# Optimization experiments

Hardware: AMD Instinct MI355X
Metric: run time of the kernel (lower is better)

The kernel has to match this reference:

```python
import jax, jax.numpy as jnp
import numpy as np

N, E, IN = 100000, 1600000, 128
H, C = 4, 16            # heads, out_channels
HID = H * C             # concat output dim = 64
SLOPE = 0.2             # GATv2Conv negative_slope default
EPS = 1e-5              # LayerNorm eps


def setup_inputs() -> dict:
    key = jax.random.key(0)
    ks = jax.random.split(key, 12)
    s = 0.05
    x = jax.random.normal(ks[0], (N, IN), jnp.float32)
    edge_index = jax.random.randint(ks[1], (2, E), 0, N, dtype=jnp.int32)
    return {
        "x": x,
        "edge_index": edge_index,
        # GATv2Conv params (lin_l: source, lin_r: target; both with bias)
        "W_l": jax.random.normal(ks[2], (IN, HID), jnp.float32) * s,
        "b_l": jnp.zeros((HID,), jnp.float32),
        "W_r": jax.random.normal(ks[3], (IN, HID), jnp.float32) * s,
        "b_r": jnp.zeros((HID,), jnp.float32),
        "att": jax.random.normal(ks[4], (H, C), jnp.float32) * s,
        "bias": jnp.zeros((HID,), jnp.float32),
        # residual projection Linear(in, heads*out, bias=False)
        "W_res": jax.random.normal(ks[5], (IN, HID), jnp.float32) * s,
        # pyg LayerNorm affine params
        "ln_w": jnp.ones((HID,), jnp.float32),
        "ln_b": jnp.zeros((HID,), jnp.float32),
    }


def reference(x, edge_index, W_l, b_l, W_r, b_r, att, bias, W_res, ln_w, ln_b):
    n = x.shape[0]
    # GATv2Conv adds self-loops by default
    loops = jnp.arange(n, dtype=edge_index.dtype)
    src = jnp.concatenate([edge_index[0], loops])  # message source j
    dst = jnp.concatenate([edge_index[1], loops])  # message target i

    xl = (x @ W_l + b_l).reshape(n, H, C)  # source-side projection
    xr = (x @ W_r + b_r).reshape(n, H, C)  # target-side projection

    # GATv2 attention: e_ij = att . LeakyReLU(xl_j + xr_i)
    e = jax.nn.leaky_relu(xl[src] + xr[dst], SLOPE)   # [Et, H, C]
    score = jnp.einsum('ehc,hc->eh', e, att)          # [Et, H]

    # segment softmax over incoming edges of each target node
    smax = jax.ops.segment_max(score, dst, num_segments=n)
    ex = jnp.exp(score - smax[dst])
    ssum = jax.ops.segment_sum(ex, dst, num_segments=n)
    alpha = ex / (ssum[dst] + 1e-16)                  # [Et, H]

    # weighted scatter-add of source features, concat heads
    msg = xl[src] * alpha[..., None]                  # [Et, H, C]
    out = jax.ops.segment_sum(msg, dst, num_segments=n).reshape(n, HID)
    out = out + bias + x @ W_res                      # bias + residual

    # pyg.nn.LayerNorm(mode='graph', batch=None): global mean/std over all elems
    out = out - out.mean()
    out = out / (out.std() + EPS)
    return out * ln_w + ln_b
```

## Files before the change

### kernel.cpp

```cpp
#include <hip/hip_runtime.h>
#include <math.h>

#define SLOPE  0.2f
#define LN_EPS 1e-5f
#define HID    64
#define IN_DIM 128
#define BM     64

__global__ __launch_bounds__(256) void proj_kernel(
    const float* __restrict__ x,
    const float* __restrict__ Wl, const float* __restrict__ bl,
    const float* __restrict__ Wr, const float* __restrict__ br,
    const float* __restrict__ Wres,
    float* __restrict__ xl, float* __restrict__ xr, float* __restrict__ out_un,
    int n)
{
    __shared__ float xs[BM][132];
    int t = threadIdx.x;
    int row0 = blockIdx.x * BM;

#pragma unroll
    for (int p = 0; p < 8; ++p) {
        int f  = t + p * 256;
        int r  = f >> 5;
        int c4 = f & 31;
        float4 v = make_float4(0.f, 0.f, 0.f, 0.f);
        if (row0 + r < n) v = ((const float4*)x)[(long)(row0 + r) * 32 + c4];
        *(float4*)&xs[r][c4 * 4] = v;
    }
    __syncthreads();

    int cb = (t & 15) * 4;
    int ry = (t >> 4) * 4;

    float4 acc[3][4];
#pragma unroll
    for (int r = 0; r < 4; ++r) {
        acc[0][r] = *(const float4*)&bl[cb];
        acc[1][r] = *(const float4*)&br[cb];
        acc[2][r] = make_float4(0.f, 0.f, 0.f, 0.f);
    }

    for (int k4 = 0; k4 < 32; ++k4) {
        float4 xv[4];
#pragma unroll
        for (int r = 0; r < 4; ++r)
            xv[r] = *(const float4*)&xs[ry + r][k4 * 4];
#pragma unroll
        for (int kk = 0; kk < 4; ++kk) {
            int k = k4 * 4 + kk;
            float4 w0 = *(const float4*)&Wl  [k * HID + cb];
            float4 w1 = *(const float4*)&Wr  [k * HID + cb];
            float4 w2 = *(const float4*)&Wres[k * HID + cb];
#pragma unroll
            for (int r = 0; r < 4; ++r) {
                float xvk = (kk == 0) ? xv[r].x : (kk == 1) ? xv[r].y
                          : (kk == 2) ? xv[r].z : xv[r].w;
                acc[0][r].x = fmaf(xvk, w0.x, acc[0][r].x);
                acc[0][r].y = fmaf(xvk, w0.y, acc[0][r].y);
                acc[0][r].z = fmaf(xvk, w0.z, acc[0][r].z);
                acc[0][r].w = fmaf(xvk, w0.w, acc[0][r].w);
                acc[1][r].x = fmaf(xvk, w1.x, acc[1][r].x);
                acc[1][r].y = fmaf(xvk, w1.y, acc[1][r].y);
                acc[1][r].z = fmaf(xvk, w1.z, acc[1][r].z);
                acc[1][r].w = fmaf(xvk, w1.w, acc[1][r].w);
                acc[2][r].x = fmaf(xvk, w2.x, acc[2][r].x);
                acc[2][r].y = fmaf(xvk, w2.y, acc[2][r].y);
                acc[2][r].z = fmaf(xvk, w2.z, acc[2][r].z);
                acc[2][r].w = fmaf(xvk, w2.w, acc[2][r].w);
            }
        }
    }

#pragma unroll
    for (int r = 0; r < 4; ++r) {
        long ro = row0 + ry + r;
        if (ro < n) {
            *(float4*)&xl    [ro * HID + cb] = acc[0][r];
            *(float4*)&xr    [ro * HID + cb] = acc[1][r];
            *(float4*)&out_un[ro * HID + cb] = acc[2][r];
        }
    }
}

__global__ void deg_init_kernel(int* __restrict__ deg, int n) {
    for (int i = blockIdx.x * blockDim.x + threadIdx.x; i < n; i += gridDim.x * blockDim.x)
        deg[i] = 1;
}

__global__ void deg_count_kernel(const int* __restrict__ dst, int* __restrict__ deg, int e) {
    for (int i = blockIdx.x * blockDim.x + threadIdx.x; i < e; i += gridDim.x * blockDim.x)
        atomicAdd(&deg[dst[i]], 1);
}

__global__ __launch_bounds__(1024) void scan_kernel(
    const int* __restrict__ deg, int* __restrict__ off, int* __restrict__ cursor, int n)
{
    __shared__ int wsum[16];
    __shared__ int carry_s;
    int t = threadIdx.x, lane = t & 63, w = t >> 6;
    if (t == 0) carry_s = 0;
    __syncthreads();
    for (int base = 0; base < n; base += 4096) {
        int i0 = base + t * 4;
        int4 v = make_int4(0, 0, 0, 0);
        if (i0 + 3 < n)      v = *(const int4*)&deg[i0];
        else if (i0 < n) {
            v.x = deg[i0];
            if (i0 + 1 < n) v.y = deg[i0 + 1];
            if (i0 + 2 < n) v.z = deg[i0 + 2];
        }
        int local = v.x + v.y + v.z + v.w;
        int inc = local;
#pragma unroll
        for (int d = 1; d < 64; d <<= 1) {
            int o = __shfl_up(inc, d, 64);
            if (lane >= d) inc += o;
        }
        if (lane == 63) wsum[w] = inc;
        __syncthreads();
        if (w == 0 && lane < 16) {
            int s = wsum[lane];
#pragma unroll
            for (int d = 1; d < 16; d <<= 1) {
                int o = __shfl_up(s, d, 16);
                if (lane >= d) s += o;
            }
            wsum[lane] = s;
        }
        __syncthreads();
        int woff = (w > 0) ? wsum[w - 1] : 0;
        int bc = carry_s;
        __syncthreads();
        int o0 = bc + woff + inc - local;
        int o1 = o0 + v.x, o2 = o1 + v.y, o3 = o2 + v.z;
        if (i0     < n) { off[i0]     = o0; cursor[i0]     = o0; }
        if (i0 + 1 < n) { off[i0 + 1] = o1; cursor[i0 + 1] = o1; }
        if (i0 + 2 < n) { off[i0 + 2] = o2; cursor[i0 + 2] = o2; }
        if (i0 + 3 < n) { off[i0 + 3] = o3; cursor[i0 + 3] = o3; }
        if (t == 1023) carry_s = bc + wsum[15];
        __syncthreads();
    }
    if (threadIdx.x == 0) off[n] = carry_s;
}

__global__ void scatter_kernel(const int* __restrict__ src, const int* __restrict__ dst,
                               int* __restrict__ cursor, int* __restrict__ csr,
                               int e, int n)
{
    int total = e + n;
    for (int i = blockIdx.x * blockDim.x + threadIdx.x; i < total; i += gridDim.x * blockDim.x) {
        int d, s;
        if (i < e) { d = dst[i]; s = src[i]; }
        else       { d = i - e;  s = i - e; }
        int p = atomicAdd(&cursor[d], 1);
        csr[p] = s;
    }
}

__global__ void init_red_kernel(double* red) {
    red[0] = 0.0; red[1] = 0.0;
}

__global__ __launch_bounds__(256) void attn_kernel(
    const float* __restrict__ xl, const float* __restrict__ xr,
    const float* __restrict__ att, const float* __restrict__ bias,
    const int* __restrict__ off, const int* __restrict__ csr,
    float* __restrict__ out_un,
    float2* __restrict__ partials, int n)
{
    int lane = threadIdx.x & 63;
    int wid  = threadIdx.x >> 6;
    int node = blockIdx.x * 4 + wid;

    float s1 = 0.0f, s2 = 0.0f;
    if (node < n) {
        float a    = att[lane];
        float bi   = bias[lane];
        float xr_v = xr[(long)node * HID + lane];

        int e0 = off[node], e1 = off[node + 1];

        float m = -INFINITY, ssum = 0.0f, acc = 0.0f;

#define ATT_UPDATE(vv)                                                    \
        {                                                                 \
            float tt = (vv) + xr_v;                                       \
            tt = (tt > 0.0f) ? tt : SLOPE * tt;                           \
            float pp = tt * a;                                            \
            pp += __shfl_xor(pp, 1, 16);                                  \
            pp += __shfl_xor(pp, 2, 16);                                  \
            pp += __shfl_xor(pp, 4, 16);                                  \
            pp += __shfl_xor(pp, 8, 16);                                  \
            float nm = fmaxf(m, pp);                                      \
            float eo = __expf(m - nm);                                    \
            float pe = __expf(pp - nm);                                   \
            acc  = acc * eo + pe * (vv);                                  \
            ssum = ssum * eo + pe;                                        \
            m = nm;                                                       \
        }

        int e = e0;
        for (; e + 4 <= e1; e += 4) {
            int j0 = csr[e], j1 = csr[e + 1], j2 = csr[e + 2], j3 = csr[e + 3];
            float v0 = xl[(long)j0 * HID + lane];
            float v1 = xl[(long)j1 * HID + lane];
            float v2 = xl[(long)j2 * HID + lane];
            float v3 = xl[(long)j3 * HID + lane];
            ATT_UPDATE(v0); ATT_UPDATE(v1); ATT_UPDATE(v2); ATT_UPDATE(v3);
        }
        for (; e < e1; ++e) {
            int j = csr[e];
            float v = xl[(long)j * HID + lane];
            ATT_UPDATE(v);
        }
#undef ATT_UPDATE

        float r = acc / (ssum + 1e-16f) + bi + out_un[(long)node * HID + lane];
        out_un[(long)node * HID + lane] = r;
        s1 = r; s2 = r * r;
    }

#pragma unroll
    for (int d = 32; d; d >>= 1) {
        s1 += __shfl_xor(s1, d, 64);
        s2 += __shfl_xor(s2, d, 64);
    }
    __shared__ float bs[8];
    if (lane == 0) { bs[wid] = s1; bs[4 + wid] = s2; }
    __syncthreads();
    if (threadIdx.x == 0)
        partials[blockIdx.x] = make_float2(bs[0] + bs[1] + bs[2] + bs[3],
                                           bs[4] + bs[5] + bs[6] + bs[7]);
}

__global__ __launch_bounds__(256) void reduce_kernel(
    const float2* __restrict__ partials, double* __restrict__ red, int nb)
{
    double a = 0.0, b = 0.0;
    for (int i = blockIdx.x * blockDim.x + threadIdx.x; i < nb; i += gridDim.x * blockDim.x) {
        float2 p = partials[i];
        a += (double)p.x; b += (double)p.y;
    }
#pragma unroll
    for (int d = 32; d; d >>= 1) {
        a += __shfl_xor(a, d, 64);
        b += __shfl_xor(b, d, 64);
    }
    if ((threadIdx.x & 63) == 0) {
        atomicAdd(&red[0], a);
        atomicAdd(&red[1], b);
    }
}

__global__ void ln_kernel(const float* __restrict__ out_un, const double* __restrict__ red,
                          const float* __restrict__ ln_w, const float* __restrict__ ln_b,
                          float* __restrict__ out, int total )
{
    double cnt  = (double)total;
    double mu   = red[0] / cnt;
    double var  = red[1] / cnt - mu * mu;
    float mean  = (float)mu;
    float inv   = 1.0f / (sqrtf((float)(var > 0.0 ? var : 0.0)) + LN_EPS);
    int n4 = total >> 2;
    for (int i = blockIdx.x * blockDim.x + threadIdx.x; i < n4; i += gridDim.x * blockDim.x) {
        float4 v = ((const float4*)out_un)[i];
        int cb = (i << 2) & 63;
        float4 r;
        r.x = (v.x - mean) * inv * ln_w[cb + 0] + ln_b[cb + 0];
        r.y = (v.y - mean) * inv * ln_w[cb + 1] + ln_b[cb + 1];
        r.z = (v.z - mean) * inv * ln_w[cb + 2] + ln_b[cb + 2];
        r.w = (v.w - mean) * inv * ln_w[cb + 3] + ln_b[cb + 3];
        ((float4*)out)[i] = r;
    }
}

extern "C" void kernel_launch(void* const* d_in, const int* in_sizes, int n_in,
                              void* d_out, int out_size, void* d_ws, size_t ws_size,
                              hipStream_t stream)
{
    const float* x    = (const float*)d_in[0];
    const int*   ei   = (const int*)d_in[1];
    const float* Wl   = (const float*)d_in[2];
    const float* bl   = (const float*)d_in[3];
    const float* Wr   = (const float*)d_in[4];
    const float* br   = (const float*)d_in[5];
    const float* att  = (const float*)d_in[6];
    const float* bias = (const float*)d_in[7];
    const float* Wres = (const float*)d_in[8];
    const float* lnw  = (const float*)d_in[9];
    const float* lnb  = (const float*)d_in[10];

    int n = in_sizes[0] / IN_DIM;
    int e = in_sizes[1] / 2;
    const int* src = ei;
    const int* dst = ei + e;

    int nblocks = (n + 3) / 4;

    char* w = (char*)d_ws;
    double* red    = (double*)w;
    float* xl      = (float*)(w + 256);
    float* xr      = xl + (long)n * HID;
    float* out_un  = xr + (long)n * HID;
    int*   deg     = (int*)(out_un + (long)n * HID);
    int*   off     = deg + n;
    int*   cursor  = off + n + 1;
    int*   csr     = cursor + n;
    float2* partials = (float2*)(csr + e + n);

    proj_kernel<<<(n + BM - 1) / BM, 256, 0, stream>>>(x, Wl, bl, Wr, br, Wres,
                                                       xl, xr, out_un, n);

    deg_init_kernel<<<512, 256, 0, stream>>>(deg, n);
    deg_count_kernel<<<4096, 256, 0, stream>>>(dst, deg, e);
    scan_kernel<<<1, 1024, 0, stream>>>(deg, off, cursor, n);
    scatter_kernel<<<4096, 256, 0, stream>>>(src, dst, cursor, csr, e, n);

    init_red_kernel<<<1, 1, 0, stream>>>(red);
    attn_kernel<<<nblocks, 256, 0, stream>>>(xl, xr, att, bias, off, csr,
                                             out_un, partials, n);
    reduce_kernel<<<64, 256, 0, stream>>>(partials, red, nblocks);

    ln_kernel<<<4096, 256, 0, stream>>>(out_un, red, lnw, lnb, (float*)d_out, n * HID);
}
```

Baseline: 577.9 us.

## Build CSR with atomic ranks instead of second atomic scatter pass

CSR construction now records each edge's rank in its destination during the degree count. A separate placement pass then writes edges using offset plus rank with no atomics, and self-loops are placed at the end of each segment. This removes one full pass of contended atomics on the cursor array. It also drops the cursor array, reuses the out_un and deg buffers for rank and partials, and replaces the multi-block atomic reduction with a single-block reduction that writes the totals directly. The costs are an extra rank-array write and read, plus a deterministic but single-block final reduction.

```diff
diff --git a/kernel.cpp b/kernel.cpp
--- a/kernel.cpp
+++ b/kernel.cpp
@@ -83,18 +83,31 @@
     }
 }
 
-__global__ void deg_init_kernel(int* __restrict__ deg, int n) {
+__global__ void deg_zero_kernel(int* __restrict__ deg, int n) {
     for (int i = blockIdx.x * blockDim.x + threadIdx.x; i < n; i += gridDim.x * blockDim.x)
-        deg[i] = 1;
-}
-
-__global__ void deg_count_kernel(const int* __restrict__ dst, int* __restrict__ deg, int e) {
-    for (int i = blockIdx.x * blockDim.x + threadIdx.x; i < e; i += gridDim.x * blockDim.x)
-        atomicAdd(&deg[dst[i]], 1);
+        deg[i] = 0;
+}
+
+__global__ __launch_bounds__(256) void rank_kernel(
+    const int* __restrict__ dst, int* __restrict__ deg, int* __restrict__ rank, int e)
+{
+    int tid = blockIdx.x * blockDim.x + threadIdx.x;
+    int stride = gridDim.x * blockDim.x;
+    int e4 = e >> 2;
+    for (int i = tid; i < e4; i += stride) {
+        int4 d = ((const int4*)dst)[i];
+        int r0 = atomicAdd(&deg[d.x], 1);
+        int r1 = atomicAdd(&deg[d.y], 1);
+        int r2 = atomicAdd(&deg[d.z], 1);
+        int r3 = atomicAdd(&deg[d.w], 1);
+        ((int4*)rank)[i] = make_int4(r0, r1, r2, r3);
+    }
+    for (int i = (e4 << 2) + tid; i < e; i += stride)
+        rank[i] = atomicAdd(&deg[dst[i]], 1);
 }
 
 __global__ __launch_bounds__(1024) void scan_kernel(
-    const int* __restrict__ deg, int* __restrict__ off, int* __restrict__ cursor, int n)
+    const int* __restrict__ deg, int* __restrict__ off, int n)
 {
     __shared__ int wsum[16];
     __shared__ int carry_s;
@@ -104,11 +117,13 @@
     for (int base = 0; base < n; base += 4096) {
         int i0 = base + t * 4;
         int4 v = make_int4(0, 0, 0, 0);
-        if (i0 + 3 < n)      v = *(const int4*)&deg[i0];
-        else if (i0 < n) {
-            v.x = deg[i0];
-            if (i0 + 1 < n) v.y = deg[i0 + 1];
-            if (i0 + 2 < n) v.z = deg[i0 + 2];
+        if (i0 + 3 < n) {
+            int4 dv = *(const int4*)&deg[i0];
+            v = make_int4(dv.x + 1, dv.y + 1, dv.z + 1, dv.w + 1);
+        } else if (i0 < n) {
+            v.x = deg[i0] + 1;
+            if (i0 + 1 < n) v.y = deg[i0 + 1] + 1;
+            if (i0 + 2 < n) v.z = deg[i0 + 2] + 1;
         }
         int local = v.x + v.y + v.z + v.w;
         int inc = local;
@@ -134,32 +149,43 @@
         __syncthreads();
         int o0 = bc + woff + inc - local;
         int o1 = o0 + v.x, o2 = o1 + v.y, o3 = o2 + v.z;
-        if (i0     < n) { off[i0]     = o0; cursor[i0]     = o0; }
-        if (i0 + 1 < n) { off[i0 + 1] = o1; cursor[i0 + 1] = o1; }
-        if (i0 + 2 < n) { off[i0 + 2] = o2; cursor[i0 + 2] = o2; }
-        if (i0 + 3 < n) { off[i0 + 3] = o3; cursor[i0 + 3] = o3; }
+        if (i0     < n) off[i0]     = o0;
+        if (i0 + 1 < n) off[i0 + 1] = o1;
+        if (i0 + 2 < n) off[i0 + 2] = o2;
+        if (i0 + 3 < n) off[i0 + 3] = o3;
         if (t == 1023) carry_s = bc + wsum[15];
         __syncthreads();
     }
     if (threadIdx.x == 0) off[n] = carry_s;
 }
 
-__global__ void scatter_kernel(const int* __restrict__ src, const int* __restrict__ dst,
-                               int* __restrict__ cursor, int* __restrict__ csr,
-                               int e, int n)
-{
-    int total = e + n;
-    for (int i = blockIdx.x * blockDim.x + threadIdx.x; i < total; i += gridDim.x * blockDim.x) {
-        int d, s;
-        if (i < e) { d = dst[i]; s = src[i]; }
-        else       { d = i - e;  s = i - e; }
-        int p = atomicAdd(&cursor[d], 1);
-        csr[p] = s;
-    }
-}
-
-__global__ void init_red_kernel(double* red) {
-    red[0] = 0.0; red[1] = 0.0;
+__global__ __launch_bounds__(256) void place_kernel(
+    const int* __restrict__ src, const int* __restrict__ dst,
+    const int* __restrict__ rank, const int* __restrict__ off,
+    int* __restrict__ csr, int e)
+{
+    int tid = blockIdx.x * blockDim.x + threadIdx.x;
+    int stride = gridDim.x * blockDim.x;
+    int e4 = e >> 2;
+    for (int i = tid; i < e4; i += stride) {
+        int4 d = ((const int4*)dst)[i];
+        int4 s = ((const int4*)src)[i];
+        int4 r = ((const int4*)rank)[i];
+        int o0 = off[d.x], o1 = off[d.y], o2 = off[d.z], o3 = off[d.w];
+        csr[o0 + r.x] = s.x;
+        csr[o1 + r.y] = s.y;
+        csr[o2 + r.z] = s.z;
+        csr[o3 + r.w] = s.w;
+    }
+    for (int i = (e4 << 2) + tid; i < e; i += stride)
+        csr[off[dst[i]] + rank[i]] = src[i];
+}
+
+__global__ void selfloop_kernel(const int* __restrict__ off, const int* __restrict__ deg,
+                                int* __restrict__ csr, int n)
+{
+    for (int i = blockIdx.x * blockDim.x + threadIdx.x; i < n; i += gridDim.x * blockDim.x)
+        csr[off[i] + deg[i]] = i;
 }
 
 __global__ __launch_bounds__(256) void attn_kernel(
@@ -234,11 +260,11 @@
                                            bs[4] + bs[5] + bs[6] + bs[7]);
 }
 
-__global__ __launch_bounds__(256) void reduce_kernel(
+__global__ __launch_bounds__(1024) void reduce_kernel(
     const float2* __restrict__ partials, double* __restrict__ red, int nb)
 {
     double a = 0.0, b = 0.0;
-    for (int i = blockIdx.x * blockDim.x + threadIdx.x; i < nb; i += gridDim.x * blockDim.x) {
+    for (int i = threadIdx.x; i < nb; i += 1024) {
         float2 p = partials[i];
         a += (double)p.x; b += (double)p.y;
     }
@@ -247,9 +273,15 @@
         a += __shfl_xor(a, d, 64);
         b += __shfl_xor(b, d, 64);
     }
-    if ((threadIdx.x & 63) == 0) {
-        atomicAdd(&red[0], a);
-        atomicAdd(&red[1], b);
+    __shared__ double sa[16], sb[16];
+    int w = threadIdx.x >> 6;
+    if ((threadIdx.x & 63) == 0) { sa[w] = a; sb[w] = b; }
+    __syncthreads();
+    if (threadIdx.x == 0) {
+        double ta = 0.0, tb = 0.0;
+#pragma unroll
+        for (int k = 0; k < 16; ++k) { ta += sa[k]; tb += sb[k]; }
+        red[0] = ta; red[1] = tb;
     }
 }
 
@@ -305,22 +337,22 @@
     float* out_un  = xr + (long)n * HID;
     int*   deg     = (int*)(out_un + (long)n * HID);
     int*   off     = deg + n;
-    int*   cursor  = off + n + 1;
-    int*   csr     = cursor + n;
-    float2* partials = (float2*)(csr + e + n);
+    int*   csr     = off + n + 1;
+    int*    rank     = (int*)out_un;
+    float2* partials = (float2*)deg;
+
+    deg_zero_kernel<<<512, 256, 0, stream>>>(deg, n);
+    rank_kernel<<<1024, 256, 0, stream>>>(dst, deg, rank, e);
+    scan_kernel<<<1, 1024, 0, stream>>>(deg, off, n);
+    place_kernel<<<1024, 256, 0, stream>>>(src, dst, rank, off, csr, e);
+    selfloop_kernel<<<512, 256, 0, stream>>>(off, deg, csr, n);
 
     proj_kernel<<<(n + BM - 1) / BM, 256, 0, stream>>>(x, Wl, bl, Wr, br, Wres,
                                                        xl, xr, out_un, n);
 
-    deg_init_kernel<<<512, 256, 0, stream>>>(deg, n);
-    deg_count_kernel<<<4096, 256, 0, stream>>>(dst, deg, e);
-    scan_kernel<<<1, 1024, 0, stream>>>(deg, off, cursor, n);
-    scatter_kernel<<<4096, 256, 0, stream>>>(src, dst, cursor, csr, e, n);
-
-    init_red_kernel<<<1, 1, 0, stream>>>(red);
     attn_kernel<<<nblocks, 256, 0, stream>>>(xl, xr, att, bias, off, csr,
                                              out_un, partials, n);
-    reduce_kernel<<<64, 256, 0, stream>>>(partials, red, nblocks);
+    reduce_kernel<<<1, 1024, 0, stream>>>(partials, red, nblocks);
 
     ln_kernel<<<4096, 256, 0, stream>>>(out_un, red, lnw, lnb, (float*)d_out, n * HID);
 }
```

Measured after the change: 462.8 us. -19.9%, faster.
